# Kernel tuning notes

Measured on AMD Instinct MI355X. Metric: run time of the kernel, lower is better.

The kernel has to match this reference:

```python
import jax, jax.numpy as jnp
import numpy as np

VOCAB, EMB, ENC_H, DEC_H, ATTN = 32000, 512, 512, 1024, 512
B, S = 64, 128
ENC2 = 2 * ENC_H


def setup_inputs() -> dict:
    key = jax.random.key(0)
    ks = jax.random.split(key, 14)
    s = 0.02
    return {
        "input_token": jax.random.randint(ks[0], (B,), 0, VOCAB),
        "hidden": jax.random.normal(ks[1], (B, DEC_H), jnp.float32),
        "cell": jax.random.normal(ks[2], (B, DEC_H), jnp.float32),
        "encoder_outputs": jax.random.normal(ks[3], (S, B, ENC2), jnp.float32),
        "mask": jnp.ones((B, S), jnp.int32),
        "embedding": jax.random.normal(ks[4], (VOCAB, EMB), jnp.float32) * s,
        "W_enc": jax.random.normal(ks[5], (ATTN, ENC2), jnp.float32) * s,
        "W_dec": jax.random.normal(ks[6], (ATTN, DEC_H), jnp.float32) * s,
        "v_attn": jax.random.normal(ks[7], (ATTN,), jnp.float32) * s,
        "W_ih": jax.random.normal(ks[8], (4 * DEC_H, EMB + ENC2), jnp.float32) * s,
        "W_hh": jax.random.normal(ks[9], (4 * DEC_H, DEC_H), jnp.float32) * s,
        "b_ih": jnp.zeros((4 * DEC_H,), jnp.float32),
        "b_hh": jnp.zeros((4 * DEC_H,), jnp.float32),
        "W_out": jax.random.normal(ks[10], (VOCAB, DEC_H + ENC2 + EMB), jnp.float32) * s,
        "b_out": jnp.zeros((VOCAB,), jnp.float32),
    }


def reference(input_token, hidden, cell, encoder_outputs, mask,
              embedding, W_enc, W_dec, v_attn, W_ih, W_hh, b_ih, b_hh,
              W_out, b_out):
    # Embedding with padding_idx=0 (row 0 zeroed in torch; emulate by zeroing lookup)
    embedded = embedding[input_token]                                # [B, EMB]
    embedded = jnp.where((input_token == 0)[:, None], 0.0, embedded)
    # Dropout in eval mode -> identity

    # Bahdanau attention
    enc_proj = jnp.einsum('sbe,ae->sba', encoder_outputs, W_enc)      # [S, B, ATTN]
    dec_proj = hidden @ W_dec.T                                       # [B, ATTN]
    scores = jnp.einsum('sba,a->sb', jnp.tanh(enc_proj + dec_proj[None]), v_attn)
    scores = scores.T                                                 # [B, S]
    scores = jnp.where(mask == 0, -jnp.inf, scores)
    attn_w = jax.nn.softmax(scores, axis=1)                           # [B, S]
    context = jnp.einsum('bs,sbe->be', attn_w, encoder_outputs)       # [B, ENC2]

    # LSTMCell (torch gate order: i, f, g, o)
    x = jnp.concatenate([embedded, context], axis=1)                  # [B, EMB+ENC2]
    gates = x @ W_ih.T + b_ih + hidden @ W_hh.T + b_hh                # [B, 4*DEC_H]
    i, f, g, o = jnp.split(gates, 4, axis=1)
    i, f, o = jax.nn.sigmoid(i), jax.nn.sigmoid(f), jax.nn.sigmoid(o)
    g = jnp.tanh(g)
    new_cell = f * cell + i * g
    new_hidden = o * jnp.tanh(new_cell)

    # Output projection
    out_in = jnp.concatenate([new_hidden, context, embedded], axis=1)
    output = out_in @ W_out.T + b_out                                 # [B, VOCAB]
    return output, new_hidden, new_cell, attn_w
```

## Files before the change

kernel.cpp:

```cpp
#include <hip/hip_runtime.h>

#define VOCAB 32000
#define EMB   512
#define ENC2  1024
#define DECH  1024
#define ATTN  512
#define BB    64
#define SS    128
#define KXH   2560
#define KOI   2560

typedef __attribute__((ext_vector_type(4))) float  f32x4;
typedef __attribute__((ext_vector_type(8))) __bf16 bf16x8;

#define OFF_DP 0
#define OFF_SC 131072
#define OFF_GP 163840
#define OFF_XH 4358144
#define OFF_OI 4685824
#define OFF_WE 5013504

static __device__ __forceinline__ bf16x8 cvt8(const float* p) {
    f32x4 a = *(const f32x4*)p;
    f32x4 b = *(const f32x4*)(p + 4);
    bf16x8 t;
    t[0] = (__bf16)a[0]; t[1] = (__bf16)a[1]; t[2] = (__bf16)a[2]; t[3] = (__bf16)a[3];
    t[4] = (__bf16)b[0]; t[5] = (__bf16)b[1]; t[6] = (__bf16)b[2]; t[7] = (__bf16)b[3];
    return t;
}

static __device__ __forceinline__ f32x4 mfma16(bf16x8 a, bf16x8 b, f32x4 c) {
    return __builtin_amdgcn_mfma_f32_16x16x32_bf16(a, b, c, 0, 0, 0);
}

__global__ void k_cvt_we(const float* __restrict__ We, __bf16* __restrict__ we16) {
    int g = blockIdx.x * 256 + threadIdx.x;
    int base = g * 8;
    *(bf16x8*)(we16 + base) = cvt8(We + base);
}

__global__ void k_prep(const int* __restrict__ tok, const float* __restrict__ hidden,
                       const float* __restrict__ emb,
                       __bf16* __restrict__ xh, __bf16* __restrict__ oi) {
    int b = blockIdx.x, t = threadIdx.x;
    int tk = tok[b];
    #pragma unroll
    for (int j = 0; j < 2; ++j) {
        int e = t + 256 * j;
        float v = (tk == 0) ? 0.f : emb[tk * EMB + e];
        __bf16 h = (__bf16)v;
        xh[b * KXH + e] = h;
        oi[b * KOI + 2048 + e] = h;
    }
    #pragma unroll
    for (int j = 0; j < 4; ++j) {
        int hidx = t + 256 * j;
        xh[b * KXH + 1536 + hidx] = (__bf16)hidden[b * DECH + hidx];
    }
}

__global__ void k_decproj(const float* __restrict__ hidden, const float* __restrict__ Wd,
                          float* __restrict__ dp) {
    int g = blockIdx.x * 256 + threadIdx.x;
    int b = g >> 9, a = g & 511;
    const float* h = hidden + b * DECH;
    const float* w = Wd + a * DECH;
    float acc = 0.f;
    #pragma unroll 4
    for (int k = 0; k < DECH; ++k) acc += h[k] * w[k];
    dp[b * ATTN + a] = acc;
}

__global__ __launch_bounds__(256) void k_scores(const float* __restrict__ enc,
                                                const __bf16* __restrict__ we16,
                                                const float* __restrict__ dp,
                                                const float* __restrict__ v,
                                                float* __restrict__ sc) {
    int t = threadIdx.x;
    int w = t >> 6, l = t & 63, lo = l & 15, hi = l >> 4;
    int r0 = blockIdx.x * 16;
    int cb = w * 128;
    f32x4 acc[8];
    #pragma unroll
    for (int f = 0; f < 8; ++f) acc[f] = (f32x4){0.f, 0.f, 0.f, 0.f};

    const float* arow = enc + (r0 + lo) * ENC2 + hi * 8;
    for (int k0 = 0; k0 < ENC2; k0 += 32) {
        bf16x8 af = cvt8(arow + k0);
        #pragma unroll
        for (int f = 0; f < 8; ++f) {
            bf16x8 bf = *(const bf16x8*)(we16 + (cb + f * 16 + lo) * ENC2 + k0 + hi * 8);
            acc[f] = mfma16(af, bf, acc[f]);
        }
    }
    int s_ = r0 >> 6;
    float p[4] = {0.f, 0.f, 0.f, 0.f};
    #pragma unroll
    for (int f = 0; f < 8; ++f) {
        int c = cb + f * 16 + lo;
        float vv = v[c];
        #pragma unroll
        for (int ri = 0; ri < 4; ++ri) {
            int r = r0 + hi * 4 + ri;
            int b = r & 63;
            p[ri] += vv * tanhf(acc[f][ri] + dp[b * ATTN + c]);
        }
    }
    #pragma unroll
    for (int m = 1; m < 16; m <<= 1) {
        #pragma unroll
        for (int ri = 0; ri < 4; ++ri) p[ri] += __shfl_xor(p[ri], m);
    }
    if (lo == 0) {
        #pragma unroll
        for (int ri = 0; ri < 4; ++ri) {
            int r = r0 + hi * 4 + ri;
            atomicAdd(&sc[(r & 63) * SS + s_], p[ri]);
        }
    }
}

__global__ void k_softmax(const float* __restrict__ sc, const int* __restrict__ mask,
                          float* __restrict__ attn) {
    int b = blockIdx.x, l = threadIdx.x;
    float s0 = sc[b * SS + l], s1 = sc[b * SS + 64 + l];
    if (mask[b * SS + l] == 0)      s0 = -3.0e38f;
    if (mask[b * SS + 64 + l] == 0) s1 = -3.0e38f;
    float m = fmaxf(s0, s1);
    #pragma unroll
    for (int x = 32; x >= 1; x >>= 1) m = fmaxf(m, __shfl_xor(m, x));
    float e0 = expf(s0 - m), e1 = expf(s1 - m);
    float sum = e0 + e1;
    #pragma unroll
    for (int x = 32; x >= 1; x >>= 1) sum += __shfl_xor(sum, x);
    float inv = 1.f / sum;
    attn[b * SS + l] = e0 * inv;
    attn[b * SS + 64 + l] = e1 * inv;
}

__global__ void k_context(const float* __restrict__ enc, const float* __restrict__ attn,
                          __bf16* __restrict__ xh, __bf16* __restrict__ oi) {
    int b = blockIdx.x, t = threadIdx.x;
    __shared__ float w[SS];
    if (t < SS) w[t] = attn[b * SS + t];
    __syncthreads();
    float acc[4] = {0.f, 0.f, 0.f, 0.f};
    for (int s = 0; s < SS; ++s) {
        float ws = w[s];
        const float* e = enc + (s * BB + b) * ENC2;
        #pragma unroll
        for (int j = 0; j < 4; ++j) acc[j] += ws * e[t + 256 * j];
    }
    #pragma unroll
    for (int j = 0; j < 4; ++j) {
        int e = t + 256 * j;
        __bf16 h = (__bf16)acc[j];
        xh[b * KXH + 512 + e] = h;
        oi[b * KOI + 1024 + e] = h;
    }
}

__global__ __launch_bounds__(256) void k_gates(const __bf16* __restrict__ xh,
                                               const float* __restrict__ Wih,
                                               const float* __restrict__ Whh,
                                               float* __restrict__ gp) {
    int bx = blockIdx.x, ks = blockIdx.y;
    int t = threadIdx.x, w = t >> 6, l = t & 63, lo = l & 15, hi = l >> 4;
    int n = bx * 64 + w * 16 + lo;
    f32x4 acc[4];
    #pragma unroll
    for (int m = 0; m < 4; ++m) acc[m] = (f32x4){0.f, 0.f, 0.f, 0.f};
    int kend = ks * 640 + 640;
    for (int k0 = ks * 640; k0 < kend; k0 += 32) {
        int k = k0 + hi * 8;
        const float* bp = (k0 < 1536) ? (Wih + n * 1536 + k) : (Whh + n * 1024 + (k - 1536));
        bf16x8 bf = cvt8(bp);
        #pragma unroll
        for (int m = 0; m < 4; ++m) {
            bf16x8 af = *(const bf16x8*)(xh + (m * 16 + lo) * KXH + k);
            acc[m] = mfma16(af, bf, acc[m]);
        }
    }
    float* out = gp + ks * (BB * 4096);
    #pragma unroll
    for (int m = 0; m < 4; ++m)
        #pragma unroll
        for (int ri = 0; ri < 4; ++ri) {
            int row = m * 16 + hi * 4 + ri;
            out[row * 4096 + n] = acc[m][ri];
        }
}

__global__ void k_lstm(const float* __restrict__ gp, const float* __restrict__ bih,
                       const float* __restrict__ bhh, const float* __restrict__ cell,
                       float* __restrict__ nh_out, float* __restrict__ nc_out,
                       __bf16* __restrict__ oi) {
    int b = blockIdx.x, t = threadIdx.x;
    #pragma unroll
    for (int j = 0; j < 4; ++j) {
        int h = t + 256 * j;
        float gi = 0.f, gf = 0.f, gg = 0.f, go = 0.f;
        #pragma unroll
        for (int ks = 0; ks < 4; ++ks) {
            const float* g = gp + ks * (BB * 4096) + b * 4096;
            gi += g[h]; gf += g[1024 + h]; gg += g[2048 + h]; go += g[3072 + h];
        }
        gi += bih[h] + bhh[h];
        gf += bih[1024 + h] + bhh[1024 + h];
        gg += bih[2048 + h] + bhh[2048 + h];
        go += bih[3072 + h] + bhh[3072 + h];
        float i_ = 1.f / (1.f + expf(-gi));
        float f_ = 1.f / (1.f + expf(-gf));
        float o_ = 1.f / (1.f + expf(-go));
        float g_ = tanhf(gg);
        float nc = f_ * cell[b * DECH + h] + i_ * g_;
        float nh = o_ * tanhf(nc);
        nc_out[b * DECH + h] = nc;
        nh_out[b * DECH + h] = nh;
        oi[b * KOI + h] = (__bf16)nh;
    }
}

__global__ __launch_bounds__(256) void k_out(const __bf16* __restrict__ oi,
                                             const float* __restrict__ Wo,
                                             const float* __restrict__ bo,
                                             float* __restrict__ out) {
    int bx = blockIdx.x;
    int t = threadIdx.x, w = t >> 6, l = t & 63, lo = l & 15, hi = l >> 4;
    int n = bx * 64 + w * 16 + lo;
    f32x4 acc[4];
    #pragma unroll
    for (int m = 0; m < 4; ++m) acc[m] = (f32x4){0.f, 0.f, 0.f, 0.f};
    const float* wrow = Wo + (long)n * KOI;
    for (int k0 = 0; k0 < KOI; k0 += 32) {
        int k = k0 + hi * 8;
        bf16x8 bf = cvt8(wrow + k);
        #pragma unroll
        for (int m = 0; m < 4; ++m) {
            bf16x8 af = *(const bf16x8*)(oi + (m * 16 + lo) * KOI + k);
            acc[m] = mfma16(af, bf, acc[m]);
        }
    }
    float bb = bo[n];
    #pragma unroll
    for (int m = 0; m < 4; ++m)
        #pragma unroll
        for (int ri = 0; ri < 4; ++ri) {
            int row = m * 16 + hi * 4 + ri;
            out[row * VOCAB + n] = acc[m][ri] + bb;
        }
}

extern "C" void kernel_launch(void* const* d_in, const int* in_sizes, int n_in,
                              void* d_out, int out_size, void* d_ws, size_t ws_size,
                              hipStream_t stream) {
    const int*   tok    = (const int*)d_in[0];
    const float* hidden = (const float*)d_in[1];
    const float* cell   = (const float*)d_in[2];
    const float* enc    = (const float*)d_in[3];
    const int*   mask   = (const int*)d_in[4];
    const float* emb    = (const float*)d_in[5];
    const float* We     = (const float*)d_in[6];
    const float* Wd     = (const float*)d_in[7];
    const float* v      = (const float*)d_in[8];
    const float* Wih    = (const float*)d_in[9];
    const float* Whh    = (const float*)d_in[10];
    const float* bih    = (const float*)d_in[11];
    const float* bhh    = (const float*)d_in[12];
    const float* Wo     = (const float*)d_in[13];
    const float* bo     = (const float*)d_in[14];

    char* ws = (char*)d_ws;
    float*  dp   = (float*)(ws + OFF_DP);
    float*  sc   = (float*)(ws + OFF_SC);
    float*  gp   = (float*)(ws + OFF_GP);
    __bf16* xh   = (__bf16*)(ws + OFF_XH);
    __bf16* oi   = (__bf16*)(ws + OFF_OI);
    __bf16* we16 = (__bf16*)(ws + OFF_WE);

    float* out_logits = (float*)d_out;
    float* nh   = out_logits + BB * VOCAB;
    float* nc   = nh + BB * DECH;
    float* attn = nc + BB * DECH;

    hipMemsetAsync(sc, 0, BB * SS * sizeof(float), stream);
    k_cvt_we<<<256, 256, 0, stream>>>(We, we16);
    k_prep<<<BB, 256, 0, stream>>>(tok, hidden, emb, xh, oi);
    k_decproj<<<128, 256, 0, stream>>>(hidden, Wd, dp);
    k_scores<<<512, 256, 0, stream>>>(enc, we16, dp, v, sc);
    k_softmax<<<BB, 64, 0, stream>>>(sc, mask, attn);
    k_context<<<BB, 256, 0, stream>>>(enc, attn, xh, oi);
    dim3 g2(64, 4);
    k_gates<<<g2, 256, 0, stream>>>(xh, Wih, Whh, gp);
    k_lstm<<<BB, 256, 0, stream>>>(gp, bih, bhh, cell, nh, nc, oi);
    k_out<<<500, 256, 0, stream>>>(oi, Wo, bo, out_logits);
}
```

Measured before the change: 733.8 us.

## Fuse prep kernels, MFMA decoder projection, wider scores tiles, split-S context

Three setup kernels (W_enc conversion, embedding/hidden prep, decoder projection) are merged into one launch, and the decoder projection moves from a scalar dot-product loop to bf16 MFMA. The scores kernel now processes 32 rows per block so each W_enc fragment feeds two MFMAs. The context reduction is split over four sequence slices with atomic accumulation, followed by a small finalize kernel. Together these cut launch count and per-block latency, at the cost of extra atomics, an extra kernel, and bf16 rounding in the decoder projection.

```diff
diff --git a/kernel.cpp b/kernel.cpp
--- a/kernel.cpp
+++ b/kernel.cpp
@@ -13,12 +13,12 @@
 typedef __attribute__((ext_vector_type(4))) float  f32x4;
 typedef __attribute__((ext_vector_type(8))) __bf16 bf16x8;
 
-#define OFF_DP 0
-#define OFF_SC 131072
-#define OFF_GP 163840
-#define OFF_XH 4358144
-#define OFF_OI 4685824
-#define OFF_WE 5013504
+#define OFF_SC  0
+#define OFF_CTX 32768
+#define OFF_GP  294912
+#define OFF_XH  4489216
+#define OFF_OI  4816896
+#define OFF_WE  5144576
 
 static __device__ __forceinline__ bf16x8 cvt8(const float* p) {
     f32x4 a = *(const f32x4*)p;
@@ -33,42 +33,59 @@
     return __builtin_amdgcn_mfma_f32_16x16x32_bf16(a, b, c, 0, 0, 0);
 }
 
-__global__ void k_cvt_we(const float* __restrict__ We, __bf16* __restrict__ we16) {
-    int g = blockIdx.x * 256 + threadIdx.x;
-    int base = g * 8;
-    *(bf16x8*)(we16 + base) = cvt8(We + base);
-}
-
-__global__ void k_prep(const int* __restrict__ tok, const float* __restrict__ hidden,
-                       const float* __restrict__ emb,
-                       __bf16* __restrict__ xh, __bf16* __restrict__ oi) {
-    int b = blockIdx.x, t = threadIdx.x;
-    int tk = tok[b];
-    #pragma unroll
-    for (int j = 0; j < 2; ++j) {
-        int e = t + 256 * j;
-        float v = (tk == 0) ? 0.f : emb[tk * EMB + e];
-        __bf16 h = (__bf16)v;
-        xh[b * KXH + e] = h;
-        oi[b * KOI + 2048 + e] = h;
-    }
-    #pragma unroll
-    for (int j = 0; j < 4; ++j) {
-        int hidx = t + 256 * j;
-        xh[b * KXH + 1536 + hidx] = (__bf16)hidden[b * DECH + hidx];
-    }
-}
-
-__global__ void k_decproj(const float* __restrict__ hidden, const float* __restrict__ Wd,
-                          float* __restrict__ dp) {
-    int g = blockIdx.x * 256 + threadIdx.x;
-    int b = g >> 9, a = g & 511;
-    const float* h = hidden + b * DECH;
-    const float* w = Wd + a * DECH;
-    float acc = 0.f;
-    #pragma unroll 4
-    for (int k = 0; k < DECH; ++k) acc += h[k] * w[k];
-    dp[b * ATTN + a] = acc;
+__global__ __launch_bounds__(256) void k_init(const float* __restrict__ We,
+                                              __bf16* __restrict__ we16,
+                                              const int* __restrict__ tok,
+                                              const float* __restrict__ hidden,
+                                              const float* __restrict__ emb,
+                                              __bf16* __restrict__ xh,
+                                              __bf16* __restrict__ oi,
+                                              const float* __restrict__ Wd,
+                                              float* __restrict__ dp) {
+    int bid = blockIdx.x, t = threadIdx.x;
+    if (bid < 256) {
+        int base = (bid * 256 + t) * 8;
+        *(bf16x8*)(we16 + base) = cvt8(We + base);
+    } else if (bid < 320) {
+        int b = bid - 256;
+        int tk = tok[b];
+        #pragma unroll
+        for (int j = 0; j < 2; ++j) {
+            int e = t + 256 * j;
+            float v = (tk == 0) ? 0.f : emb[tk * EMB + e];
+            __bf16 h = (__bf16)v;
+            xh[b * KXH + e] = h;
+            oi[b * KOI + 2048 + e] = h;
+        }
+        #pragma unroll
+        for (int j = 0; j < 4; ++j) {
+            int hidx = t + 256 * j;
+            xh[b * KXH + 1536 + hidx] = (__bf16)hidden[b * DECH + hidx];
+        }
+    } else {
+        int bx = bid - 320;
+        int w = t >> 6, l = t & 63, lo = l & 15, hi = l >> 4;
+        int n = bx * 64 + w * 16 + lo;
+        f32x4 acc[4];
+        #pragma unroll
+        for (int m = 0; m < 4; ++m) acc[m] = (f32x4){0.f, 0.f, 0.f, 0.f};
+        for (int k0 = 0; k0 < DECH; k0 += 32) {
+            int k = k0 + hi * 8;
+            bf16x8 bf = cvt8(Wd + n * DECH + k);
+            #pragma unroll
+            for (int m = 0; m < 4; ++m) {
+                bf16x8 af = cvt8(hidden + (m * 16 + lo) * DECH + k);
+                acc[m] = mfma16(af, bf, acc[m]);
+            }
+        }
+        #pragma unroll
+        for (int m = 0; m < 4; ++m)
+            #pragma unroll
+            for (int ri = 0; ri < 4; ++ri) {
+                int b = m * 16 + hi * 4 + ri;
+                dp[b * ATTN + n] = acc[m][ri];
+            }
+    }
 }
 
 __global__ __launch_bounds__(256) void k_scores(const float* __restrict__ enc,
@@ -78,45 +95,56 @@
                                                 float* __restrict__ sc) {
     int t = threadIdx.x;
     int w = t >> 6, l = t & 63, lo = l & 15, hi = l >> 4;
-    int r0 = blockIdx.x * 16;
+    int r0 = blockIdx.x * 32;
     int cb = w * 128;
-    f32x4 acc[8];
-    #pragma unroll
-    for (int f = 0; f < 8; ++f) acc[f] = (f32x4){0.f, 0.f, 0.f, 0.f};
-
-    const float* arow = enc + (r0 + lo) * ENC2 + hi * 8;
+    f32x4 acc[2][8];
+    #pragma unroll
+    for (int m = 0; m < 2; ++m)
+        #pragma unroll
+        for (int f = 0; f < 8; ++f) acc[m][f] = (f32x4){0.f, 0.f, 0.f, 0.f};
+
+    const float* arow0 = enc + (r0 + lo) * ENC2 + hi * 8;
+    const float* arow1 = enc + (r0 + 16 + lo) * ENC2 + hi * 8;
     for (int k0 = 0; k0 < ENC2; k0 += 32) {
-        bf16x8 af = cvt8(arow + k0);
+        bf16x8 a0 = cvt8(arow0 + k0);
+        bf16x8 a1 = cvt8(arow1 + k0);
         #pragma unroll
         for (int f = 0; f < 8; ++f) {
             bf16x8 bf = *(const bf16x8*)(we16 + (cb + f * 16 + lo) * ENC2 + k0 + hi * 8);
-            acc[f] = mfma16(af, bf, acc[f]);
+            acc[0][f] = mfma16(a0, bf, acc[0][f]);
+            acc[1][f] = mfma16(a1, bf, acc[1][f]);
         }
     }
     int s_ = r0 >> 6;
-    float p[4] = {0.f, 0.f, 0.f, 0.f};
+    float p[2][4] = {{0.f,0.f,0.f,0.f},{0.f,0.f,0.f,0.f}};
     #pragma unroll
     for (int f = 0; f < 8; ++f) {
         int c = cb + f * 16 + lo;
         float vv = v[c];
         #pragma unroll
-        for (int ri = 0; ri < 4; ++ri) {
-            int r = r0 + hi * 4 + ri;
-            int b = r & 63;
-            p[ri] += vv * tanhf(acc[f][ri] + dp[b * ATTN + c]);
-        }
-    }
-    #pragma unroll
-    for (int m = 1; m < 16; m <<= 1) {
-        #pragma unroll
-        for (int ri = 0; ri < 4; ++ri) p[ri] += __shfl_xor(p[ri], m);
+        for (int m = 0; m < 2; ++m)
+            #pragma unroll
+            for (int ri = 0; ri < 4; ++ri) {
+                int r = r0 + m * 16 + hi * 4 + ri;
+                int b = r & 63;
+                p[m][ri] += vv * tanhf(acc[m][f][ri] + dp[b * ATTN + c]);
+            }
+    }
+    #pragma unroll
+    for (int x = 1; x < 16; x <<= 1) {
+        #pragma unroll
+        for (int m = 0; m < 2; ++m)
+            #pragma unroll
+            for (int ri = 0; ri < 4; ++ri) p[m][ri] += __shfl_xor(p[m][ri], x);
     }
     if (lo == 0) {
         #pragma unroll
-        for (int ri = 0; ri < 4; ++ri) {
-            int r = r0 + hi * 4 + ri;
-            atomicAdd(&sc[(r & 63) * SS + s_], p[ri]);
-        }
+        for (int m = 0; m < 2; ++m)
+            #pragma unroll
+            for (int ri = 0; ri < 4; ++ri) {
+                int r = r0 + m * 16 + hi * 4 + ri;
+                atomicAdd(&sc[(r & 63) * SS + s_], p[m][ri]);
+            }
     }
 }
 
@@ -138,23 +166,32 @@
     attn[b * SS + 64 + l] = e1 * inv;
 }
 
-__global__ void k_context(const float* __restrict__ enc, const float* __restrict__ attn,
-                          __bf16* __restrict__ xh, __bf16* __restrict__ oi) {
-    int b = blockIdx.x, t = threadIdx.x;
-    __shared__ float w[SS];
-    if (t < SS) w[t] = attn[b * SS + t];
+__global__ __launch_bounds__(256) void k_context(const float* __restrict__ enc,
+                                                 const float* __restrict__ attn,
+                                                 float* __restrict__ ctx) {
+    int b = blockIdx.x & 63, sl = blockIdx.x >> 6, t = threadIdx.x;
+    __shared__ float w[32];
+    if (t < 32) w[t] = attn[b * SS + sl * 32 + t];
     __syncthreads();
     float acc[4] = {0.f, 0.f, 0.f, 0.f};
-    for (int s = 0; s < SS; ++s) {
-        float ws = w[s];
+    for (int si = 0; si < 32; ++si) {
+        int s = sl * 32 + si;
+        float ws = w[si];
         const float* e = enc + (s * BB + b) * ENC2;
         #pragma unroll
         for (int j = 0; j < 4; ++j) acc[j] += ws * e[t + 256 * j];
     }
+    #pragma unroll
+    for (int j = 0; j < 4; ++j) atomicAdd(&ctx[b * ENC2 + t + 256 * j], acc[j]);
+}
+
+__global__ void k_ctxfin(const float* __restrict__ ctx,
+                         __bf16* __restrict__ xh, __bf16* __restrict__ oi) {
+    int b = blockIdx.x, t = threadIdx.x;
     #pragma unroll
     for (int j = 0; j < 4; ++j) {
         int e = t + 256 * j;
-        __bf16 h = (__bf16)acc[j];
+        __bf16 h = (__bf16)ctx[b * ENC2 + e];
         xh[b * KXH + 512 + e] = h;
         oi[b * KOI + 1024 + e] = h;
     }
@@ -271,25 +308,25 @@
     const float* bo     = (const float*)d_in[14];
 
     char* ws = (char*)d_ws;
-    float*  dp   = (float*)(ws + OFF_DP);
     float*  sc   = (float*)(ws + OFF_SC);
+    float*  ctx  = (float*)(ws + OFF_CTX);
     float*  gp   = (float*)(ws + OFF_GP);
     __bf16* xh   = (__bf16*)(ws + OFF_XH);
     __bf16* oi   = (__bf16*)(ws + OFF_OI);
     __bf16* we16 = (__bf16*)(ws + OFF_WE);
+    float*  dp   = (float*)(ws + OFF_WE + 1048576);
 
     float* out_logits = (float*)d_out;
     float* nh   = out_logits + BB * VOCAB;
     float* nc   = nh + BB * DECH;
     float* attn = nc + BB * DECH;
 
-    hipMemsetAsync(sc, 0, BB * SS * sizeof(float), stream);
-    k_cvt_we<<<256, 256, 0, stream>>>(We, we16);
-    k_prep<<<BB, 256, 0, stream>>>(tok, hidden, emb, xh, oi);
-    k_decproj<<<128, 256, 0, stream>>>(hidden, Wd, dp);
-    k_scores<<<512, 256, 0, stream>>>(enc, we16, dp, v, sc);
+    hipMemsetAsync(sc, 0, (BB * SS + BB * ENC2) * sizeof(float), stream);
+    k_init<<<328, 256, 0, stream>>>(We, we16, tok, hidden, emb, xh, oi, Wd, dp);
+    k_scores<<<256, 256, 0, stream>>>(enc, we16, dp, v, sc);
     k_softmax<<<BB, 64, 0, stream>>>(sc, mask, attn);
-    k_context<<<BB, 256, 0, stream>>>(enc, attn, xh, oi);
+    k_context<<<256, 256, 0, stream>>>(enc, attn, ctx);
+    k_ctxfin<<<BB, 256, 0, stream>>>(ctx, xh, oi);
     dim3 g2(64, 4);
     k_gates<<<g2, 256, 0, stream>>>(xh, Wih, Whh, gp);
     k_lstm<<<BB, 256, 0, stream>>>(gp, bih, bhh, cell, nh, nc, oi);
```

Result: faster. 683.8 us (-6.8%).
